# Optimization experiments

Measured on AMD Instinct MI355X. Metric: run time of the kernel, lower is better.

## Reference

```python
import jax, jax.numpy as jnp
import numpy as np

N = 100000   # nodes
E = 1600000  # edges
DIN, DH, DOUT = 64, 128, 128


def setup_inputs() -> dict:
    key = jax.random.key(0)
    ks = jax.random.split(key, 12)
    x = jax.random.normal(ks[0], (N, DIN), dtype=jnp.float32)
    edge_index = jax.random.randint(ks[1], (2, E), 0, N, dtype=jnp.int32)
    s = 1.0 / np.sqrt(DIN)
    W1 = jax.random.uniform(ks[2], (DIN, DH), jnp.float32, -s, s)
    b1 = jnp.zeros((DH,), jnp.float32)
    g1 = jnp.ones((DH,), jnp.float32)
    bt1 = jnp.zeros((DH,), jnp.float32)
    s2 = 1.0 / np.sqrt(DH)
    W2 = jax.random.uniform(ks[3], (DH, DOUT), jnp.float32, -s2, s2)
    b2 = jnp.zeros((DOUT,), jnp.float32)
    g2 = jnp.ones((DOUT,), jnp.float32)
    bt2 = jnp.zeros((DOUT,), jnp.float32)
    return {"x": x, "edge_index": edge_index, "W1": W1, "b1": b1, "g1": g1,
            "bt1": bt1, "W2": W2, "b2": b2, "g2": g2, "bt2": bt2}


def _layer_norm(h, g, b, eps=1e-5):
    mu = h.mean(-1, keepdims=True)
    var = h.var(-1, keepdims=True)
    return (h - mu) * jax.lax.rsqrt(var + eps) * g + b


def reference(x, edge_index, W1, b1, g1, bt1, W2, b2, g2, bt2):
    # GCN normalization with self-loops (shared graph structure for both layers)
    src, dst = edge_index[0], edge_index[1]
    loops = jnp.arange(N, dtype=src.dtype)
    src = jnp.concatenate([src, loops])
    dst = jnp.concatenate([dst, loops])
    deg = jax.ops.segment_sum(jnp.ones_like(src, jnp.float32), dst, num_segments=N)
    dinv = jnp.where(deg > 0, jax.lax.rsqrt(deg), 0.0)
    norm = dinv[src] * dinv[dst]  # [E+N]

    def gcn(h, W, b):
        hw = h @ W                         # linear first (PyG GCNConv)
        msg = hw[src] * norm[:, None]      # gather + edge scale
        return jax.ops.segment_sum(msg, dst, num_segments=N) + b

    h = jax.nn.relu(_layer_norm(gcn(x, W1, b1), g1, bt1))
    # dropout is identity at inference
    h = jax.nn.relu(_layer_norm(gcn(h, W2, b2), g2, bt2))
    return h
```

## Files before the change

kernel.cpp:

```cpp
#include <hip/hip_runtime.h>

#define NN 100000
#define NE 1600000
#define NBKT 196
#define CAP 12288
#define EPB 8192
#define ABLK ((NE + EPB - 1) / EPB)
typedef unsigned short u16;
typedef unsigned int u32;

typedef __attribute__((ext_vector_type(8))) short short8v;
typedef __attribute__((ext_vector_type(4))) float f32x4;

__device__ __forceinline__ u32 f2bf(float f) {
    u32 u = __float_as_uint(f);
    return (u + 0x7fffu + ((u >> 16) & 1u)) >> 16;
}
__device__ __forceinline__ u32 pack2(float a, float b) {
    return f2bf(a) | (f2bf(b) << 16);
}
__device__ __forceinline__ void accum8(float* a, uint4 u, float w) {
    a[0] += __uint_as_float(u.x << 16) * w;
    a[1] += __uint_as_float(u.x & 0xffff0000u) * w;
    a[2] += __uint_as_float(u.y << 16) * w;
    a[3] += __uint_as_float(u.y & 0xffff0000u) * w;
    a[4] += __uint_as_float(u.z << 16) * w;
    a[5] += __uint_as_float(u.z & 0xffff0000u) * w;
    a[6] += __uint_as_float(u.w << 16) * w;
    a[7] += __uint_as_float(u.w & 0xffff0000u) * w;
}

__global__ __launch_bounds__(256) void kA_bin(const int* __restrict__ src,
                                              const int* __restrict__ dst,
                                              int* __restrict__ gcnt,
                                              u32* __restrict__ binned) {
    __shared__ int bc[NBKT];
    __shared__ int cbase[NBKT];
    const int tid = threadIdx.x;
    for (int i = tid; i < NBKT; i += 256) bc[i] = 0;
    __syncthreads();
    const int e0 = blockIdx.x * EPB;
#pragma unroll
    for (int i = 0; i < EPB / 256; ++i) {
        const int e = e0 + i * 256 + tid;
        if (e < NE) atomicAdd(&bc[dst[e] >> 9], 1);
    }
    __syncthreads();
    for (int i = tid; i < NBKT; i += 256)
        cbase[i] = bc[i] ? atomicAdd(&gcnt[i], bc[i]) : 0;
    __syncthreads();
    for (int i = tid; i < NBKT; i += 256) bc[i] = 0;
    __syncthreads();
#pragma unroll
    for (int i = 0; i < EPB / 256; ++i) {
        const int e = e0 + i * 256 + tid;
        if (e < NE) {
            const int d = dst[e];
            const int bkt = d >> 9;
            const int p = atomicAdd(&bc[bkt], 1);
            binned[bkt * CAP + cbase[bkt] + p] = ((u32)src[e] << 9) | (u32)(d & 511);
        }
    }
}

__global__ __launch_bounds__(256) void kB_fill(const u32* __restrict__ binned,
                                               const int* __restrict__ gcnt,
                                               int2* __restrict__ off2,
                                               float* __restrict__ dinv,
                                               int* __restrict__ csr) {
    __shared__ int lcnt[512];
    __shared__ int lpos[512];
    __shared__ int ws[4];
    const int b = blockIdx.x;
    const int tid = threadIdx.x;
    const int cnt = gcnt[b];
    const int base0 = b * CAP;
    const int node0 = b << 9;
    lcnt[tid] = 0;
    lcnt[tid + 256] = 0;
    __syncthreads();
    for (int e = tid; e < cnt; e += 256)
        atomicAdd(&lcnt[binned[base0 + e] & 511], 1);
    __syncthreads();
    const int c0 = lcnt[tid * 2], c1 = lcnt[tid * 2 + 1];
    const int s = c0 + c1;
    const int lane = tid & 63, w = tid >> 6;
    int incl = s;
#pragma unroll
    for (int o = 1; o < 64; o <<= 1) {
        const int u = __shfl_up(incl, o);
        if (lane >= o) incl += u;
    }
    if (lane == 63) ws[w] = incl;
    __syncthreads();
    int base = incl - s;
    for (int i = 0; i < w; ++i) base += ws[i];
    lpos[tid * 2] = base;
    lpos[tid * 2 + 1] = base + c0;
    const int n0 = node0 + tid * 2;
    if (n0 < NN) {
        off2[n0] = make_int2(base0 + base, base0 + base + c0);
        dinv[n0] = rsqrtf(1.0f + (float)c0);
    }
    if (n0 + 1 < NN) {
        off2[n0 + 1] = make_int2(base0 + base + c0, base0 + base + c0 + c1);
        dinv[n0 + 1] = rsqrtf(1.0f + (float)c1);
    }
    __syncthreads();
    for (int e = tid; e < cnt; e += 256) {
        const u32 u = binned[base0 + e];
        const int p = atomicAdd(&lpos[u & 511], 1);
        csr[base0 + p] = (int)(u >> 9);
    }
}

__global__ __launch_bounds__(256) void k_prep(const float* __restrict__ W1,
                                              const float* __restrict__ W2,
                                              u16* __restrict__ WT1,
                                              u16* __restrict__ WT2,
                                              int* __restrict__ gcnt) {
    const int i = blockIdx.x * 256 + threadIdx.x;
    if (i < 8192) {
        const int k = i >> 7, c = i & 127;
        WT1[c * 64 + k] = (u16)f2bf(W1[i]);
    } else if (i < 24576) {
        const int i2 = i - 8192;
        const int k = i2 >> 7, c = i2 & 127;
        WT2[c * 128 + k] = (u16)f2bf(W2[i2]);
    } else if (i < 24576 + NBKT) {
        gcnt[i - 24576] = 0;
    }
}

__global__ __launch_bounds__(256) void k_cvt(const float* __restrict__ x,
                                             const float* __restrict__ dinv,
                                             u16* __restrict__ xb) {
    const int i = blockIdx.x * 256 + threadIdx.x;
    if (i < NN * 8) {
        const int row = i >> 3;
        const float dr = dinv[row];
        const float4 v0 = *(const float4*)&x[(size_t)i * 8];
        const float4 v1 = *(const float4*)&x[(size_t)i * 8 + 4];
        uint4 o;
        o.x = pack2(v0.x * dr, v0.y * dr); o.y = pack2(v0.z * dr, v0.w * dr);
        o.z = pack2(v1.x * dr, v1.y * dr); o.w = pack2(v1.z * dr, v1.w * dr);
        *(uint4*)&xb[(size_t)i * 8] = o;
    }
}

template<int K, bool FP32OUT, bool PRESCALE>
__global__ __launch_bounds__(256) void k_fused(const u16* __restrict__ A,
                                               const int2* __restrict__ off2,
                                               const int* __restrict__ csr,
                                               const float* __restrict__ dinv,
                                               const u16* __restrict__ WT,
                                               const float* __restrict__ bias,
                                               const float* __restrict__ g,
                                               const float* __restrict__ bt,
                                               void* __restrict__ outp) {
    constexpr int RB = K * 2;
    constexpr int SUBS = 512 / K;
    constexpr int LSH = (K == 64) ? 7 : 8;
    __shared__ u16 As[16 * K];
    __shared__ float s1s[4][16];
    __shared__ float s2s[4][16];
    const int tid = threadIdx.x;
    const int wv = tid >> 6, lane = tid & 63;
    const int sub = lane / (64 / SUBS);
    const int l = lane & (64 / SUBS - 1);
    const char* Ab = (const char*)A + ((u32)l << 4);
    const int nodeBase = blockIdx.x * 16 + wv * 4;

    for (int i = 0; i < 4; ++i) {
        const int node = nodeBase + i;
        const float di = dinv[node];
        float a[8] = {};
        {
            const uint4 u = *(const uint4*)(Ab + ((u32)node << LSH));
            accum8(a, u, (sub == 0) ? 1.0f : 0.0f);
        }
        const int2 oe = off2[node];
        int base = oe.x;
        const int e1 = oe.y;
        u32 iA = 0, iB = 0, iC = 0;
        float vA = 0.f, vB = 0.f, vC = 0.f;
        if (base < e1) {
            const int eA = base + sub, eB = eA + SUBS, eC = eA + 2 * SUBS;
            iA = (u32)csr[min(eA, e1 - 1)];
            iB = (u32)csr[min(eB, e1 - 1)];
            iC = (u32)csr[min(eC, e1 - 1)];
            vA = (eA < e1) ? 1.f : 0.f;
            vB = (eB < e1) ? 1.f : 0.f;
            vC = (eC < e1) ? 1.f : 0.f;
        }
        while (base < e1) {
            const uint4 uA = *(const uint4*)(Ab + (iA << LSH));
            const uint4 uB = *(const uint4*)(Ab + (iB << LSH));
            const uint4 uC = *(const uint4*)(Ab + (iC << LSH));
            const float wA = vA, wB = vB, wC = vC;
            base += 3 * SUBS;
            if (base < e1) {
                const int eA = base + sub, eB = eA + SUBS, eC = eA + 2 * SUBS;
                iA = (u32)csr[min(eA, e1 - 1)];
                iB = (u32)csr[min(eB, e1 - 1)];
                iC = (u32)csr[min(eC, e1 - 1)];
                vA = (eA < e1) ? 1.f : 0.f;
                vB = (eB < e1) ? 1.f : 0.f;
                vC = (eC < e1) ? 1.f : 0.f;
            }
            accum8(a, uA, wA);
            accum8(a, uB, wB);
            accum8(a, uC, wC);
        }
#pragma unroll
        for (int t = 0; t < 8; ++t)
#pragma unroll
            for (int o = 64 / SUBS; o < 64; o <<= 1)
                a[t] += __shfl_xor(a[t], o);
        if (sub == 0) {
            const int row = wv * 4 + i;
            uint4 o;
            o.x = pack2(a[0] * di, a[1] * di); o.y = pack2(a[2] * di, a[3] * di);
            o.z = pack2(a[4] * di, a[5] * di); o.w = pack2(a[6] * di, a[7] * di);
            *(uint4*)((char*)As + row * RB + (((u32)l << 4) ^ ((u32)(row & 7) << 4))) = o;
        }
    }
    __syncthreads();

    const int lr = lane & 15, kg = lane >> 4;
    short8v af[K / 32];
#pragma unroll
    for (int kk = 0; kk < K / 32; ++kk)
        af[kk] = *(const short8v*)((const char*)As + lr * RB +
                                   ((u32)(kk * 64 + kg * 16) ^ ((u32)(lr & 7) << 4)));
    f32x4 acc[2];
    float bv[2], gv[2], tv[2];
#pragma unroll
    for (int nt = 0; nt < 2; ++nt) {
        acc[nt] = (f32x4){0.f, 0.f, 0.f, 0.f};
        const int col = wv * 32 + nt * 16 + lr;
        short8v bf[K / 32];
#pragma unroll
        for (int kk = 0; kk < K / 32; ++kk)
            bf[kk] = *(const short8v*)&WT[col * K + kk * 32 + kg * 8];
#pragma unroll
        for (int kk = 0; kk < K / 32; ++kk)
            acc[nt] = __builtin_amdgcn_mfma_f32_16x16x32_bf16(af[kk], bf[kk], acc[nt], 0, 0, 0);
        bv[nt] = bias[col]; gv[nt] = g[col]; tv[nt] = bt[col];
    }

    float s1[4] = {0.f, 0.f, 0.f, 0.f};
    float s2[4] = {0.f, 0.f, 0.f, 0.f};
#pragma unroll
    for (int nt = 0; nt < 2; ++nt)
#pragma unroll
        for (int j = 0; j < 4; ++j) {
            const float v = acc[nt][j] + bv[nt];
            acc[nt][j] = v;
            s1[j] += v;
            s2[j] += v * v;
        }
#pragma unroll
    for (int j = 0; j < 4; ++j)
#pragma unroll
        for (int o = 1; o < 16; o <<= 1) {
            s1[j] += __shfl_xor(s1[j], o);
            s2[j] += __shfl_xor(s2[j], o);
        }
    if (lr == 0) {
#pragma unroll
        for (int j = 0; j < 4; ++j) {
            s1s[wv][kg * 4 + j] = s1[j];
            s2s[wv][kg * 4 + j] = s2[j];
        }
    }
    __syncthreads();

#pragma unroll
    for (int j = 0; j < 4; ++j) {
        const int row = kg * 4 + j;
        const float t1 = s1s[0][row] + s1s[1][row] + s1s[2][row] + s1s[3][row];
        const float t2 = s2s[0][row] + s2s[1][row] + s2s[2][row] + s2s[3][row];
        const float mu = t1 * (1.0f / 128.0f);
        const float var = t2 * (1.0f / 128.0f) - mu * mu;
        const float rs = rsqrtf(var + 1e-5f);
        const int node = blockIdx.x * 16 + row;
        const float dr = PRESCALE ? dinv[node] : 1.0f;
#pragma unroll
        for (int nt = 0; nt < 2; ++nt) {
            const float y = fmaxf((acc[nt][j] - mu) * rs * gv[nt] + tv[nt], 0.f) * dr;
            const int col = wv * 32 + nt * 16 + lr;
            if constexpr (FP32OUT)
                ((float*)outp)[(size_t)node * 128 + col] = y;
            else
                ((u16*)outp)[(size_t)node * 128 + col] = (u16)f2bf(y);
        }
    }
}

extern "C" void kernel_launch(void* const* d_in, const int* in_sizes, int n_in,
                              void* d_out, int out_size, void* d_ws, size_t ws_size,
                              hipStream_t stream) {
    const float* x   = (const float*)d_in[0];
    const int*   ei  = (const int*)d_in[1];
    const float* W1  = (const float*)d_in[2];
    const float* b1  = (const float*)d_in[3];
    const float* g1  = (const float*)d_in[4];
    const float* bt1 = (const float*)d_in[5];
    const float* W2  = (const float*)d_in[6];
    const float* b2  = (const float*)d_in[7];
    const float* g2  = (const float*)d_in[8];
    const float* bt2 = (const float*)d_in[9];

    const int* src = ei;
    const int* dst = ei + NE;

    const int NP = (NN + 255) & ~255;
    int*   gcnt   = (int*)d_ws;
    int2*  off2   = (int2*)(gcnt + 256);
    float* dinv   = (float*)(off2 + NP);
    int*   csr    = (int*)(dinv + NP);
    u32*   binned = (u32*)(csr + NBKT * CAP);
    u16*   xb     = (u16*)(binned + NBKT * CAP);
    u16*   h1     = xb + (size_t)NN * 64;
    u16*   WT1    = h1 + (size_t)NN * 128;
    u16*   WT2    = WT1 + 128 * 64;

    k_prep<<<(24576 + NBKT + 255) / 256, 256, 0, stream>>>(W1, W2, WT1, WT2, gcnt);
    kA_bin<<<ABLK, 256, 0, stream>>>(src, dst, gcnt, binned);
    kB_fill<<<NBKT, 256, 0, stream>>>(binned, gcnt, off2, dinv, csr);
    k_cvt<<<(NN * 8 + 255) / 256, 256, 0, stream>>>(x, dinv, xb);

    k_fused<64, false, true><<<NN / 16, 256, 0, stream>>>(
        xb, off2, csr, dinv, WT1, b1, g1, bt1, h1);

    k_fused<128, true, false><<<NN / 16, 256, 0, stream>>>(
        h1, off2, csr, dinv, WT2, b2, g2, bt2, d_out);
}
```

Before: 204.7 us.

## Fuse x conversion into CSR fill and give each wave full-row 16-node tiles

The separate x-to-bf16 conversion kernel is folded into the CSR fill kernel, using degree-inverse values held in shared memory, which removes one launch and a reread of dinv. The fused aggregate+GEMM kernel now has each wave handle 16 nodes and compute all 128 output columns itself, so the layer-norm statistics reduce within the wave and the block-wide __syncthreads and shared reductions go away. The binning kernel also processes fewer edges per block (EPB 8192 -> 2048), launching more blocks. In exchange each wave keeps 8 accumulator tiles in registers, which may lower occupancy, and there are 4x fewer blocks for the gather phase.

```diff
diff --git a/kernel.cpp b/kernel.cpp
--- a/kernel.cpp
+++ b/kernel.cpp
@@ -4,7 +4,7 @@
 #define NE 1600000
 #define NBKT 196
 #define CAP 12288
-#define EPB 8192
+#define EPB 2048
 #define ABLK ((NE + EPB - 1) / EPB)
 typedef unsigned short u16;
 typedef unsigned int u32;
@@ -67,9 +67,12 @@
                                                const int* __restrict__ gcnt,
                                                int2* __restrict__ off2,
                                                float* __restrict__ dinv,
-                                               int* __restrict__ csr) {
+                                               int* __restrict__ csr,
+                                               const float* __restrict__ x,
+                                               u16* __restrict__ xb) {
     __shared__ int lcnt[512];
     __shared__ int lpos[512];
+    __shared__ float sdinv[512];
     __shared__ int ws[4];
     const int b = blockIdx.x;
     const int tid = threadIdx.x;
@@ -97,20 +100,36 @@
     for (int i = 0; i < w; ++i) base += ws[i];
     lpos[tid * 2] = base;
     lpos[tid * 2 + 1] = base + c0;
+    const float d0 = rsqrtf(1.0f + (float)c0);
+    const float d1 = rsqrtf(1.0f + (float)c1);
+    sdinv[tid * 2] = d0;
+    sdinv[tid * 2 + 1] = d1;
     const int n0 = node0 + tid * 2;
     if (n0 < NN) {
         off2[n0] = make_int2(base0 + base, base0 + base + c0);
-        dinv[n0] = rsqrtf(1.0f + (float)c0);
+        dinv[n0] = d0;
     }
     if (n0 + 1 < NN) {
         off2[n0 + 1] = make_int2(base0 + base + c0, base0 + base + c0 + c1);
-        dinv[n0 + 1] = rsqrtf(1.0f + (float)c1);
+        dinv[n0 + 1] = d1;
     }
     __syncthreads();
     for (int e = tid; e < cnt; e += 256) {
         const u32 u = binned[base0 + e];
         const int p = atomicAdd(&lpos[u & 511], 1);
         csr[base0 + p] = (int)(u >> 9);
+    }
+    const int nmax = min(512, NN - node0);
+    for (int gi = tid; gi < nmax * 8; gi += 256) {
+        const int nl = gi >> 3, ch = gi & 7;
+        const float dr = sdinv[nl];
+        const size_t xo = (size_t)(node0 + nl) * 64 + ch * 8;
+        const float4 v0 = *(const float4*)&x[xo];
+        const float4 v1 = *(const float4*)&x[xo + 4];
+        uint4 o;
+        o.x = pack2(v0.x * dr, v0.y * dr); o.y = pack2(v0.z * dr, v0.w * dr);
+        o.z = pack2(v1.x * dr, v1.y * dr); o.w = pack2(v1.z * dr, v1.w * dr);
+        *(uint4*)&xb[xo] = o;
     }
 }
 
@@ -132,22 +151,6 @@
     }
 }
 
-__global__ __launch_bounds__(256) void k_cvt(const float* __restrict__ x,
-                                             const float* __restrict__ dinv,
-                                             u16* __restrict__ xb) {
-    const int i = blockIdx.x * 256 + threadIdx.x;
-    if (i < NN * 8) {
-        const int row = i >> 3;
-        const float dr = dinv[row];
-        const float4 v0 = *(const float4*)&x[(size_t)i * 8];
-        const float4 v1 = *(const float4*)&x[(size_t)i * 8 + 4];
-        uint4 o;
-        o.x = pack2(v0.x * dr, v0.y * dr); o.y = pack2(v0.z * dr, v0.w * dr);
-        o.z = pack2(v1.x * dr, v1.y * dr); o.w = pack2(v1.z * dr, v1.w * dr);
-        *(uint4*)&xb[(size_t)i * 8] = o;
-    }
-}
-
 template<int K, bool FP32OUT, bool PRESCALE>
 __global__ __launch_bounds__(256) void k_fused(const u16* __restrict__ A,
                                                const int2* __restrict__ off2,
@@ -161,18 +164,17 @@
     constexpr int RB = K * 2;
     constexpr int SUBS = 512 / K;
     constexpr int LSH = (K == 64) ? 7 : 8;
-    __shared__ u16 As[16 * K];
-    __shared__ float s1s[4][16];
-    __shared__ float s2s[4][16];
+    __shared__ u16 As[4 * 16 * K];
     const int tid = threadIdx.x;
     const int wv = tid >> 6, lane = tid & 63;
     const int sub = lane / (64 / SUBS);
     const int l = lane & (64 / SUBS - 1);
     const char* Ab = (const char*)A + ((u32)l << 4);
-    const int nodeBase = blockIdx.x * 16 + wv * 4;
-
-    for (int i = 0; i < 4; ++i) {
-        const int node = nodeBase + i;
+    char* myAs = (char*)As + wv * 16 * RB;
+    const int nodeBase = blockIdx.x * 64 + wv * 16;
+
+    for (int i = 0; i < 16; ++i) {
+        const int node = min(nodeBase + i, NN - 1);
         const float di = dinv[node];
         float a[8] = {};
         {
@@ -218,27 +220,24 @@
             for (int o = 64 / SUBS; o < 64; o <<= 1)
                 a[t] += __shfl_xor(a[t], o);
         if (sub == 0) {
-            const int row = wv * 4 + i;
             uint4 o;
             o.x = pack2(a[0] * di, a[1] * di); o.y = pack2(a[2] * di, a[3] * di);
             o.z = pack2(a[4] * di, a[5] * di); o.w = pack2(a[6] * di, a[7] * di);
-            *(uint4*)((char*)As + row * RB + (((u32)l << 4) ^ ((u32)(row & 7) << 4))) = o;
-        }
-    }
-    __syncthreads();
+            *(uint4*)(myAs + i * RB + (((u32)l << 4) ^ ((u32)(i & 7) << 4))) = o;
+        }
+    }
 
     const int lr = lane & 15, kg = lane >> 4;
     short8v af[K / 32];
 #pragma unroll
     for (int kk = 0; kk < K / 32; ++kk)
-        af[kk] = *(const short8v*)((const char*)As + lr * RB +
+        af[kk] = *(const short8v*)(myAs + lr * RB +
                                    ((u32)(kk * 64 + kg * 16) ^ ((u32)(lr & 7) << 4)));
-    f32x4 acc[2];
-    float bv[2], gv[2], tv[2];
-#pragma unroll
-    for (int nt = 0; nt < 2; ++nt) {
+    f32x4 acc[8];
+#pragma unroll
+    for (int nt = 0; nt < 8; ++nt) {
         acc[nt] = (f32x4){0.f, 0.f, 0.f, 0.f};
-        const int col = wv * 32 + nt * 16 + lr;
+        const int col = nt * 16 + lr;
         short8v bf[K / 32];
 #pragma unroll
         for (int kk = 0; kk < K / 32; ++kk)
@@ -246,20 +245,21 @@
 #pragma unroll
         for (int kk = 0; kk < K / 32; ++kk)
             acc[nt] = __builtin_amdgcn_mfma_f32_16x16x32_bf16(af[kk], bf[kk], acc[nt], 0, 0, 0);
-        bv[nt] = bias[col]; gv[nt] = g[col]; tv[nt] = bt[col];
     }
 
     float s1[4] = {0.f, 0.f, 0.f, 0.f};
     float s2[4] = {0.f, 0.f, 0.f, 0.f};
 #pragma unroll
-    for (int nt = 0; nt < 2; ++nt)
+    for (int nt = 0; nt < 8; ++nt) {
+        const float bvn = bias[nt * 16 + lr];
 #pragma unroll
         for (int j = 0; j < 4; ++j) {
-            const float v = acc[nt][j] + bv[nt];
+            const float v = acc[nt][j] + bvn;
             acc[nt][j] = v;
             s1[j] += v;
             s2[j] += v * v;
         }
+    }
 #pragma unroll
     for (int j = 0; j < 4; ++j)
 #pragma unroll
@@ -267,33 +267,33 @@
             s1[j] += __shfl_xor(s1[j], o);
             s2[j] += __shfl_xor(s2[j], o);
         }
-    if (lr == 0) {
+    float mu4[4], rs4[4], dr4[4];
+    int wr4[4];
+#pragma unroll
+    for (int j = 0; j < 4; ++j) {
+        const int node = nodeBase + kg * 4 + j;
+        wr4[j] = node < NN;
+        const float mu = s1[j] * (1.0f / 128.0f);
+        const float var = s2[j] * (1.0f / 128.0f) - mu * mu;
+        mu4[j] = mu;
+        rs4[j] = rsqrtf(var + 1e-5f);
+        dr4[j] = PRESCALE ? dinv[min(node, NN - 1)] : 1.0f;
+    }
+#pragma unroll
+    for (int nt = 0; nt < 8; ++nt) {
+        const int col = nt * 16 + lr;
+        const float gvn = g[col];
+        const float tvn = bt[col];
 #pragma unroll
         for (int j = 0; j < 4; ++j) {
-            s1s[wv][kg * 4 + j] = s1[j];
-            s2s[wv][kg * 4 + j] = s2[j];
-        }
-    }
-    __syncthreads();
-
-#pragma unroll
-    for (int j = 0; j < 4; ++j) {
-        const int row = kg * 4 + j;
-        const float t1 = s1s[0][row] + s1s[1][row] + s1s[2][row] + s1s[3][row];
-        const float t2 = s2s[0][row] + s2s[1][row] + s2s[2][row] + s2s[3][row];
-        const float mu = t1 * (1.0f / 128.0f);
-        const float var = t2 * (1.0f / 128.0f) - mu * mu;
-        const float rs = rsqrtf(var + 1e-5f);
-        const int node = blockIdx.x * 16 + row;
-        const float dr = PRESCALE ? dinv[node] : 1.0f;
-#pragma unroll
-        for (int nt = 0; nt < 2; ++nt) {
-            const float y = fmaxf((acc[nt][j] - mu) * rs * gv[nt] + tv[nt], 0.f) * dr;
-            const int col = wv * 32 + nt * 16 + lr;
-            if constexpr (FP32OUT)
-                ((float*)outp)[(size_t)node * 128 + col] = y;
-            else
-                ((u16*)outp)[(size_t)node * 128 + col] = (u16)f2bf(y);
+            if (wr4[j]) {
+                const int node = nodeBase + kg * 4 + j;
+                const float y = fmaxf((acc[nt][j] - mu4[j]) * rs4[j] * gvn + tvn, 0.f) * dr4[j];
+                if constexpr (FP32OUT)
+                    ((float*)outp)[(size_t)node * 128 + col] = y;
+                else
+                    ((u16*)outp)[(size_t)node * 128 + col] = (u16)f2bf(y);
+            }
         }
     }
 }
@@ -328,12 +328,11 @@
 
     k_prep<<<(24576 + NBKT + 255) / 256, 256, 0, stream>>>(W1, W2, WT1, WT2, gcnt);
     kA_bin<<<ABLK, 256, 0, stream>>>(src, dst, gcnt, binned);
-    kB_fill<<<NBKT, 256, 0, stream>>>(binned, gcnt, off2, dinv, csr);
-    k_cvt<<<(NN * 8 + 255) / 256, 256, 0, stream>>>(x, dinv, xb);
-
-    k_fused<64, false, true><<<NN / 16, 256, 0, stream>>>(
+    kB_fill<<<NBKT, 256, 0, stream>>>(binned, gcnt, off2, dinv, csr, x, xb);
+
+    k_fused<64, false, true><<<(NN + 63) / 64, 256, 0, stream>>>(
         xb, off2, csr, dinv, WT1, b1, g1, bt1, h1);
 
-    k_fused<128, true, false><<<NN / 16, 256, 0, stream>>>(
+    k_fused<128, true, false><<<(NN + 63) / 64, 256, 0, stream>>>(
         h1, off2, csr, dinv, WT2, b2, g2, bt2, d_out);
 }
```

Measured after the change: 236.5 us. +15.6%, slower.
